# Kernel tuning notes

Measured on AMD Instinct MI355X. Metric: run time of the kernel, lower is better.

The kernel has to match this reference:

```python
import jax, jax.numpy as jnp
import numpy as np

KS = 3
K3 = KS ** 3
NUM_K = 4
KM_ITERS = 10  # fixed Lloyd iterations (original runs to tolerance)


def _unfold3d(xp, d, h, w):
    # xp: [B, C, d+2, h+2, w+2] -> [B, C, d, h, w, 27]; kernel dims flattened as (k1,k2,k3)
    sl = [xp[:, :, i:i + d, j:j + h, l:l + w]
          for i in range(KS) for j in range(KS) for l in range(KS)]
    return jnp.stack(sl, axis=-1)


def _kmeans(pts):
    # pts: [N, C]. Deterministic init with first NUM_K points, fixed Lloyd iterations.
    cent0 = pts[:NUM_K]

    def assign(cent):
        d2 = (jnp.sum(pts * pts, -1, keepdims=True)
              - 2.0 * (pts @ cent.T) + jnp.sum(cent * cent, -1))  # [N, K]
        return jnp.argmin(d2, axis=-1)

    def step(cent, _):
        oh = jax.nn.one_hot(assign(cent), NUM_K, dtype=pts.dtype)  # [N, K]
        cnt = jnp.maximum(oh.sum(0), 1.0)
        cent = (oh.T @ pts) / cnt[:, None]
        return cent, None

    cent, _ = jax.lax.scan(step, cent0, None, length=KM_ITERS)
    return assign(cent), cent


def _mlp3(z, w1, b1, w2, b2, w3, b3):
    z = jax.nn.relu(z @ w1 + b1)
    z = jax.nn.relu(z @ w2 + b2)
    return z @ w3 + b3


def reference(x, proj_w, base_w, gk_w1, gk_b1, gk_w2, gk_b2, gk_w3, gk_b3,
              gb_w1, gb_b1, gb_w2, gb_b2, gb_w3, gb_b3, prelu_a):
    b, c, d, h, w = x.shape
    o = base_w.shape[0]
    n = d * h * w
    x_in = x
    # 1x1x1 input projection (no bias)
    xp = jnp.einsum('oi,bidhw->bodhw', proj_w, x)
    xp = jnp.pad(xp, ((0, 0), (0, 0), (1, 1), (1, 1), (1, 1)))
    patches = _unfold3d(xp, d, h, w)                                # [b,c,d,h,w,27]
    # mean_type 's': mean over kernel dims -> per-voxel channel summary
    x_mean = patches.mean(-1).reshape(b, c, n).transpose(0, 2, 1)   # [b,n,c]
    idx, cent = jax.vmap(_kmeans)(x_mean)                           # [b,n], [b,K,c]
    feat = cent.reshape(b, NUM_K * c)
    # per-cluster dynamic kernel gates in (0,1)
    w_i = jax.nn.sigmoid(_mlp3(feat, gk_w1, gk_b1, gk_w2, gk_b2, gk_w3, gk_b3))
    w_i = w_i.reshape(b, NUM_K, K3).transpose(1, 0, 2)[:, :, None, None, :]  # [K,b,1,1,27]
    weight = (w_i * base_w).reshape(NUM_K, b, o, c * K3)            # [K,b,o,c*27]
    bias = _mlp3(feat, gb_w1, gb_b1, gb_w2, gb_b2, gb_w3, gb_b3)
    bias = bias.reshape(b, NUM_K, o).transpose(1, 0, 2)[..., None]  # [K,b,o,1]
    # im2col: [b, c*27, n] with (c, k) channel-major flattening as in the torch rearrange
    xf = patches.reshape(b, c, n, K3).transpose(0, 1, 3, 2).reshape(b, c * K3, n)
    out = jnp.einsum('kbof,bfn->kbon', weight, xf) + bias           # [K,b,o,n]
    mask = jax.nn.one_hot(idx, NUM_K, dtype=out.dtype)              # [b,n,K]
    out = (out * mask.transpose(2, 0, 1)[:, :, None, :]).sum(0)     # [b,o,n]
    out = out.reshape(b, o, d, h, w)
    out = jnp.where(out >= 0, out, prelu_a * out)                   # PReLU (single param)
    return out + x_in


def setup_inputs():
    key = jax.random.key(0)
    ks = jax.random.split(key, 12)
    B, C, O, D = 1, 64, 64, 40
    inner, inner2 = 128, 64
    fin = C * NUM_K

    def lin(k, i, o_):
        s = 1.0 / np.sqrt(i)
        return jax.random.uniform(k, (i, o_), jnp.float32, -s, s)

    return {
        'x': jax.random.normal(ks[0], (B, C, D, D, D), jnp.float32),
        'proj_w': jax.random.normal(ks[1], (C, C), jnp.float32) / np.sqrt(C),
        'base_w': jax.random.normal(ks[2], (O, C, K3), jnp.float32) / np.sqrt(C * K3),
        'gk_w1': lin(ks[3], fin, inner), 'gk_b1': jnp.zeros((inner,), jnp.float32),
        'gk_w2': lin(ks[4], inner, inner), 'gk_b2': jnp.zeros((inner,), jnp.float32),
        'gk_w3': lin(ks[5], inner, K3 * NUM_K), 'gk_b3': jnp.zeros((K3 * NUM_K,), jnp.float32),
        'gb_w1': lin(ks[6], fin, inner2), 'gb_b1': jnp.zeros((inner2,), jnp.float32),
        'gb_w2': lin(ks[7], inner2, inner2), 'gb_b2': jnp.zeros((inner2,), jnp.float32),
        'gb_w3': lin(ks[8], inner2, O * NUM_K), 'gb_b3': jnp.zeros((O * NUM_K,), jnp.float32),
        'prelu_a': jnp.full((1,), 0.25, jnp.float32),
    }
```

## Files before the change

kernel.cpp:

```cpp
#include <hip/hip_runtime.h>
#include <math.h>

typedef short v8s __attribute__((ext_vector_type(8)));
typedef float v4f __attribute__((ext_vector_type(4)));

#define NVOX 64000
#define NPAD 74088
#define P2   1764
#define GSTR 592704
#define NCPY 8
#define ITST (NCPY*260)

__device__ __forceinline__ unsigned short bf16rne(float f){
  unsigned int u = __float_as_uint(f);
  u += 0x7FFFu + ((u >> 16) & 1u);
  return (unsigned short)(u >> 16);
}

__global__ __launch_bounds__(256) void proj_k(const float* __restrict__ x,
                                              const float* __restrict__ pw,
                                              float* __restrict__ xp,
                                              short* __restrict__ xpt){
  int tid = threadIdx.x;
  int m = (blockIdx.x >> 1) * 256 + tid;
  int half = blockIdx.x & 1;
  float xv[64];
#pragma unroll
  for (int i = 0; i < 64; i++) xv[i] = x[(size_t)i * NVOX + m];
  int d = m / 1600; int r = m - d * 1600; int h = r / 40; int w = r - h * 40;
  int p = ((d + 1) * 42 + (h + 1)) * 42 + (w + 1);
  const float4* pw4 = (const float4*)pw;
  for (int g8 = half * 4; g8 < half * 4 + 4; g8++){
    v8s pk;
#pragma unroll
    for (int j = 0; j < 8; j++){
      int co = g8 * 8 + j;
      float acc = 0.f;
#pragma unroll
      for (int q = 0; q < 16; q++){
        float4 pv = pw4[co * 16 + q];
        acc = fmaf(pv.x, xv[4*q+0], acc);
        acc = fmaf(pv.y, xv[4*q+1], acc);
        acc = fmaf(pv.z, xv[4*q+2], acc);
        acc = fmaf(pv.w, xv[4*q+3], acc);
      }
      xp[(size_t)co * NVOX + m] = acc;
      pk[j] = (short)bf16rne(acc);
    }
    *(v8s*)(xpt + (size_t)g8 * GSTR + (size_t)p * 8) = pk;
  }
}

__global__ __launch_bounds__(256) void boxwh_k(const float* __restrict__ in,
                                               float* __restrict__ out){
  __shared__ float s0[1600], s1[1600];
  size_t base = (size_t)blockIdx.x * 1600;
  int t = threadIdx.x;
  for (int e = t; e < 1600; e += 256) s0[e] = in[base + e];
  __syncthreads();
  for (int e = t; e < 1600; e += 256){
    int w = e % 40;
    float s = s0[e];
    if (w > 0)  s += s0[e - 1];
    if (w < 39) s += s0[e + 1];
    s1[e] = s;
  }
  __syncthreads();
  for (int e = t; e < 1600; e += 256){
    int h = e / 40;
    float s = s1[e];
    if (h > 0)  s += s1[e - 40];
    if (h < 39) s += s1[e + 40];
    out[base + e] = s;
  }
}
__global__ void boxd_k(const float* __restrict__ in, float* __restrict__ out){
  int g = blockIdx.x * 256 + threadIdx.x;
  int d = (g / 1600) % 40;
  float s = in[g];
  if (d > 0)  s += in[g - 1600];
  if (d < 39) s += in[g + 1600];
  out[g] = s * (1.f / 27.f);
}

__global__ __launch_bounds__(256) void transp_k(const float* __restrict__ in,
                                                float* __restrict__ out){
  __shared__ float tile[64][65];
  int t = threadIdx.x;
  int nb = blockIdx.x * 64;
  int l = t & 63, g = t >> 6;
  for (int cc = g; cc < 64; cc += 4)
    tile[cc][l] = in[(size_t)cc * NVOX + nb + l];
  __syncthreads();
  for (int nn = g; nn < 64; nn += 4)
    out[(size_t)(nb + nn) * 64 + l] = tile[l][nn];
}

__global__ void kinit_k(const float* __restrict__ xmt, float* __restrict__ km){
  int t = threadIdx.x;
  km[t] = xmt[(size_t)(t >> 6) * 64 + (t & 63)];
  if (t < 4) km[256 + t] = 1.f;
  for (int j = 260 + t; j < 12 * ITST; j += 256) km[j] = 0.f;
}

__global__ __launch_bounds__(128) void assign_k(const float* __restrict__ xmt,
                                                const float* __restrict__ kin,
                                                float* __restrict__ kout,
                                                int* __restrict__ idx, int mode){
  __shared__ float s_cent[256];
  __shared__ float s_cc[4];
  __shared__ float s_red[260];
  __shared__ float s_x[128 * 65];
  __shared__ int   s_kb[128];
  int t = threadIdx.x, lane = t & 63, wv = t >> 6;
  for (int j = t; j < 256; j += 128){
    float sum = 0.f, cnt = 0.f;
#pragma unroll
    for (int s = 0; s < NCPY; s++){
      sum += kin[s * 260 + j];
      cnt += kin[s * 260 + 256 + (j >> 6)];
    }
    s_cent[j] = sum / fmaxf(cnt, 1.f);
  }
  for (int j = t; j < 260; j += 128) s_red[j] = 0.f;
  __syncthreads();
  if (t < 4){
    const float4* cc4 = (const float4*)(s_cent + t * 64);
    float s = 0.f;
#pragma unroll
    for (int q = 0; q < 16; q++){
      float4 v = cc4[q];
      s = fmaf(v.x, v.x, s); s = fmaf(v.y, v.y, s);
      s = fmaf(v.z, v.z, s); s = fmaf(v.w, v.w, s);
    }
    s_cc[t] = s;
  }
  __syncthreads();
  int n = blockIdx.x * 128 + t;
  const float4* xt = (const float4*)(xmt + (size_t)n * 64);
  float4 xq[16];
#pragma unroll
  for (int q = 0; q < 16; q++) xq[q] = xt[q];
  float d0 = 0.f, d1 = 0.f, d2 = 0.f, d3 = 0.f;
  const float4* c4 = (const float4*)s_cent;
#pragma unroll
  for (int q = 0; q < 16; q++){
    float4 p0 = c4[q], p1 = c4[16 + q], p2 = c4[32 + q], p3 = c4[48 + q];
    d0 = fmaf(p0.x, xq[q].x, d0); d0 = fmaf(p0.y, xq[q].y, d0);
    d0 = fmaf(p0.z, xq[q].z, d0); d0 = fmaf(p0.w, xq[q].w, d0);
    d1 = fmaf(p1.x, xq[q].x, d1); d1 = fmaf(p1.y, xq[q].y, d1);
    d1 = fmaf(p1.z, xq[q].z, d1); d1 = fmaf(p1.w, xq[q].w, d1);
    d2 = fmaf(p2.x, xq[q].x, d2); d2 = fmaf(p2.y, xq[q].y, d2);
    d2 = fmaf(p2.z, xq[q].z, d2); d2 = fmaf(p2.w, xq[q].w, d2);
    d3 = fmaf(p3.x, xq[q].x, d3); d3 = fmaf(p3.y, xq[q].y, d3);
    d3 = fmaf(p3.z, xq[q].z, d3); d3 = fmaf(p3.w, xq[q].w, d3);
  }
  float sc0 = s_cc[0] - 2.f * d0;
  float sc1 = s_cc[1] - 2.f * d1;
  float sc2 = s_cc[2] - 2.f * d2;
  float sc3 = s_cc[3] - 2.f * d3;
  int kb = 0; float bs = sc0;
  if (sc1 < bs){ bs = sc1; kb = 1; }
  if (sc2 < bs){ bs = sc2; kb = 2; }
  if (sc3 < bs){ bs = sc3; kb = 3; }
  if (mode){
    idx[n] = kb;
  } else {
    s_kb[t] = kb;
#pragma unroll
    for (int q = 0; q < 16; q++){
      s_x[t * 65 + 4*q + 0] = xq[q].x;
      s_x[t * 65 + 4*q + 1] = xq[q].y;
      s_x[t * 65 + 4*q + 2] = xq[q].z;
      s_x[t * 65 + 4*q + 3] = xq[q].w;
    }
    __syncthreads();
    float a0 = 0.f, a1 = 0.f, a2 = 0.f, a3 = 0.f;
    int rowbase = wv * 64;
#pragma unroll 16
    for (int j = 0; j < 64; j++){
      float v = s_x[(rowbase + j) * 65 + lane];
      int kj = s_kb[rowbase + j];
      a0 += (kj == 0) ? v : 0.f;
      a1 += (kj == 1) ? v : 0.f;
      a2 += (kj == 2) ? v : 0.f;
      a3 += (kj == 3) ? v : 0.f;
    }
    atomicAdd(&s_red[lane], a0);
    atomicAdd(&s_red[64 + lane], a1);
    atomicAdd(&s_red[128 + lane], a2);
    atomicAdd(&s_red[192 + lane], a3);
#pragma unroll
    for (int kk = 0; kk < 4; kk++){
      unsigned long long m = __ballot(kb == kk);
      if (lane == 0) atomicAdd(&s_red[256 + kk], (float)__popcll(m));
    }
    __syncthreads();
    float* kslot = kout + (blockIdx.x & (NCPY - 1)) * 260;
    for (int j = t; j < 260; j += 128) atomicAdd(&kslot[j], s_red[j]);
  }
}

__global__ void mlp_k(const float* __restrict__ km10,
                      const float* __restrict__ w1, const float* __restrict__ b1,
                      const float* __restrict__ w2, const float* __restrict__ b2,
                      const float* __restrict__ w3, const float* __restrict__ b3,
                      const float* __restrict__ u1, const float* __restrict__ c1,
                      const float* __restrict__ u2, const float* __restrict__ c2,
                      const float* __restrict__ u3, const float* __restrict__ c3,
                      float* __restrict__ wi, float* __restrict__ bias){
  __shared__ float s_feat[256], s_h1[128], s_h2[128], s_g1[64], s_g2[64];
  int t = threadIdx.x;
  {
    float sum = 0.f, cnt = 0.f;
#pragma unroll
    for (int s = 0; s < NCPY; s++){
      sum += km10[s * 260 + t];
      cnt += km10[s * 260 + 256 + (t >> 6)];
    }
    s_feat[t] = sum / fmaxf(cnt, 1.f);
  }
  __syncthreads();
  if (t < 128){
    float z = b1[t];
    for (int i = 0; i < 256; i++) z = fmaf(s_feat[i], w1[i * 128 + t], z);
    s_h1[t] = fmaxf(z, 0.f);
  }
  __syncthreads();
  if (t < 128){
    float z = b2[t];
    for (int i = 0; i < 128; i++) z = fmaf(s_h1[i], w2[i * 128 + t], z);
    s_h2[t] = fmaxf(z, 0.f);
  }
  __syncthreads();
  if (t < 108){
    float z = b3[t];
    for (int i = 0; i < 128; i++) z = fmaf(s_h2[i], w3[i * 108 + t], z);
    wi[t] = 1.f / (1.f + expf(-z));
  }
  if (t < 64){
    float z = c1[t];
    for (int i = 0; i < 256; i++) z = fmaf(s_feat[i], u1[i * 64 + t], z);
    s_g1[t] = fmaxf(z, 0.f);
  }
  __syncthreads();
  if (t < 64){
    float z = c2[t];
    for (int i = 0; i < 64; i++) z = fmaf(s_g1[i], u2[i * 64 + t], z);
    s_g2[t] = fmaxf(z, 0.f);
  }
  __syncthreads();
  {
    float z = c3[t];
    for (int i = 0; i < 64; i++) z = fmaf(s_g2[i], u3[i * 256 + t], z);
    bias[t] = z;
  }
}

__global__ void bwprep_k(const float* __restrict__ bw, short* __restrict__ bwb){
  int e = blockIdx.x * 256 + threadIdx.x;
  int t = e >> 12; int rem = e & 4095;
  int o = rem >> 6; int c = rem & 63;
  bwb[e] = (short)bf16rne(bw[(o * 64 + c) * 27 + t]);
}

__global__ __launch_bounds__(256) void conv_k(const short* __restrict__ xpt,
                                              const short* __restrict__ bwb,
                                              const float* __restrict__ wi,
                                              const float* __restrict__ bias,
                                              const int* __restrict__ idx,
                                              const float* __restrict__ x,
                                              const float* __restrict__ pa,
                                              float* __restrict__ out){
  static const int POFF[27] = {
    -P2-42-1, -P2-42, -P2-42+1, -P2-1, -P2, -P2+1, -P2+42-1, -P2+42, -P2+42+1,
    -42-1, -42, -42+1, -1, 0, 1, 42-1, 42, 42+1,
    P2-42-1, P2-42, P2-42+1, P2-1, P2, P2+1, P2+42-1, P2+42, P2+42+1 };
  __shared__ float s_wi[108];
  __shared__ float s_bias[256];
  __shared__ float s_acc[64 * 68];
  int tid = threadIdx.x;
  for (int j = tid; j < 108; j += 256) s_wi[j] = wi[j];
  s_bias[tid] = bias[tid];
  __syncthreads();
  int wv = tid >> 6, lane = tid & 63;
  int kc = wv & 1, mh = wv >> 1;
  int col = lane & 15, kg = lane >> 4;
  int vb = blockIdx.x * 64;
  int p4[4], ki4[4];
#pragma unroll
  for (int nt = 0; nt < 4; nt++){
    int v = vb + nt * 16 + col;
    ki4[nt] = idx[v];
    int d = v / 1600; int r = v - d * 1600; int h = r / 40; int w = r - h * 40;
    p4[nt] = ((d + 1) * 42 + (h + 1)) * 42 + (w + 1);
  }
  const short* bg = xpt + (size_t)(kc * 4 + kg) * GSTR;
  const short* bp0 = bg + (size_t)p4[0] * 8;
  const short* bp1 = bg + (size_t)p4[1] * 8;
  const short* bp2 = bg + (size_t)p4[2] * 8;
  const short* bp3 = bg + (size_t)p4[3] * 8;
  int ao0 = (mh * 32 + col) * 64 + kc * 32 + kg * 8;
  int ao1 = ao0 + 16 * 64;
  v4f acc[2][4];
#pragma unroll
  for (int m2 = 0; m2 < 2; m2++)
#pragma unroll
    for (int nt = 0; nt < 4; nt++) acc[m2][nt] = (v4f){0.f, 0.f, 0.f, 0.f};
  v4f zero = {0.f, 0.f, 0.f, 0.f};
#pragma unroll 9
  for (int t = 0; t < 27; t++){
    int po8 = POFF[t] * 8;
    v8s a0 = *(const v8s*)(bwb + t * 4096 + ao0);
    v8s a1 = *(const v8s*)(bwb + t * 4096 + ao1);
    v8s b0 = *(const v8s*)(bp0 + po8);
    v8s b1 = *(const v8s*)(bp1 + po8);
    v8s b2 = *(const v8s*)(bp2 + po8);
    v8s b3 = *(const v8s*)(bp3 + po8);
    float wk0 = s_wi[ki4[0] * 27 + t];
    float wk1 = s_wi[ki4[1] * 27 + t];
    float wk2 = s_wi[ki4[2] * 27 + t];
    float wk3 = s_wi[ki4[3] * 27 + t];
    v4f tp;
    tp = __builtin_amdgcn_mfma_f32_16x16x32_bf16(a0, b0, zero, 0, 0, 0); acc[0][0] += tp * wk0;
    tp = __builtin_amdgcn_mfma_f32_16x16x32_bf16(a1, b0, zero, 0, 0, 0); acc[1][0] += tp * wk0;
    tp = __builtin_amdgcn_mfma_f32_16x16x32_bf16(a0, b1, zero, 0, 0, 0); acc[0][1] += tp * wk1;
    tp = __builtin_amdgcn_mfma_f32_16x16x32_bf16(a1, b1, zero, 0, 0, 0); acc[1][1] += tp * wk1;
    tp = __builtin_amdgcn_mfma_f32_16x16x32_bf16(a0, b2, zero, 0, 0, 0); acc[0][2] += tp * wk2;
    tp = __builtin_amdgcn_mfma_f32_16x16x32_bf16(a1, b2, zero, 0, 0, 0); acc[1][2] += tp * wk2;
    tp = __builtin_amdgcn_mfma_f32_16x16x32_bf16(a0, b3, zero, 0, 0, 0); acc[0][3] += tp * wk3;
    tp = __builtin_amdgcn_mfma_f32_16x16x32_bf16(a1, b3, zero, 0, 0, 0); acc[1][3] += tp * wk3;
  }
  __syncthreads();
  if (kc == 1){
#pragma unroll
    for (int m2 = 0; m2 < 2; m2++)
#pragma unroll
      for (int nt = 0; nt < 4; nt++)
        *(v4f*)(&s_acc[(nt * 16 + col) * 68 + mh * 32 + m2 * 16 + kg * 4]) = acc[m2][nt];
  }
  __syncthreads();
  if (kc == 0){
    float pav = pa[0];
#pragma unroll
    for (int m2 = 0; m2 < 2; m2++){
#pragma unroll
      for (int nt = 0; nt < 4; nt++){
        v4f other = *(const v4f*)(&s_acc[(nt * 16 + col) * 68 + mh * 32 + m2 * 16 + kg * 4]);
        v4f sum = acc[m2][nt] + other;
        int n = vb + nt * 16 + col;
#pragma unroll
        for (int r = 0; r < 4; r++){
          int o = mh * 32 + m2 * 16 + kg * 4 + r;
          float val = sum[r] + s_bias[ki4[nt] * 64 + o];
          val = (val >= 0.f) ? val : pav * val;
          size_t off = (size_t)o * NVOX + n;
          out[off] = val + x[off];
        }
      }
    }
  }
}

extern "C" void kernel_launch(void* const* d_in, const int* in_sizes, int n_in,
                              void* d_out, int out_size, void* d_ws, size_t ws_size,
                              hipStream_t stream){
  const float* x    = (const float*)d_in[0];
  const float* pw   = (const float*)d_in[1];
  const float* bw   = (const float*)d_in[2];
  const float* gkw1 = (const float*)d_in[3];
  const float* gkb1 = (const float*)d_in[4];
  const float* gkw2 = (const float*)d_in[5];
  const float* gkb2 = (const float*)d_in[6];
  const float* gkw3 = (const float*)d_in[7];
  const float* gkb3 = (const float*)d_in[8];
  const float* gbw1 = (const float*)d_in[9];
  const float* gbb1 = (const float*)d_in[10];
  const float* gbw2 = (const float*)d_in[11];
  const float* gbb2 = (const float*)d_in[12];
  const float* gbw3 = (const float*)d_in[13];
  const float* gbb3 = (const float*)d_in[14];
  const float* pa   = (const float*)d_in[15];
  float* outp = (float*)d_out;

  float* ws   = (float*)d_ws;
  float* XP   = ws;
  float* BU2  = ws + 4096000;
  float* BU1  = ws + 8192000;
  short* XPT  = (short*)(ws + 12288000);
  short* BWB  = XPT + (size_t)NPAD * 64;
  float* KM   = (float*)(BWB + 110592);
  float* WI   = KM + 12 * ITST;
  float* BIAS = WI + 108;
  int*   IDX  = (int*)(BIAS + 256);
  float* XMT  = XP;

  hipMemsetAsync(XPT, 0, (size_t)NPAD * 64 * 2, stream);
  proj_k<<<500, 256, 0, stream>>>(x, pw, XP, XPT);
  boxwh_k<<<2560, 256, 0, stream>>>(XP, BU2);
  boxd_k<<<16000, 256, 0, stream>>>(BU2, BU1);
  transp_k<<<1000, 256, 0, stream>>>(BU1, XMT);
  kinit_k<<<1, 256, 0, stream>>>(XMT, KM);
  for (int i = 0; i <= 10; i++)
    assign_k<<<500, 128, 0, stream>>>(XMT, KM + i * ITST, KM + (i + 1) * ITST, IDX,
                                      (i == 10) ? 1 : 0);
  mlp_k<<<1, 256, 0, stream>>>(KM + 10 * ITST,
                               gkw1, gkb1, gkw2, gkb2, gkw3, gkb3,
                               gbw1, gbb1, gbw2, gbb2, gbw3, gbb3,
                               WI, BIAS);
  bwprep_k<<<432, 256, 0, stream>>>(bw, BWB);
  conv_k<<<1000, 256, 0, stream>>>(XPT, BWB, WI, BIAS, IDX, x, pa, outp);
}
```

Before: 332.9 us.

## Fuse k-means init and Lloyd iterations into one cooperative persistent kernel

Replaces the init kernel and the eleven separate assign launches with a single cooperative kernel of 250 blocks of 256 threads. Each thread keeps its voxel feature vector in registers and in shared memory across all iterations, and grid.sync replaces the kernel-launch boundaries between iterations. This removes per-launch overhead and the repeated reload of the point data from global memory. In exchange it uses a large shared-memory tile of about 67 KB per block, which limits occupancy. It also relies on every block being co-resident for the grid-wide barrier to work.

```diff
diff --git a/kernel.cpp b/kernel.cpp
--- a/kernel.cpp
+++ b/kernel.cpp
@@ -1,5 +1,8 @@
 #include <hip/hip_runtime.h>
+#include <hip/hip_cooperative_groups.h>
 #include <math.h>
+
+namespace cg = cooperative_groups;
 
 typedef short v8s __attribute__((ext_vector_type(8)));
 typedef float v4f __attribute__((ext_vector_type(4)));
@@ -96,108 +99,114 @@
     out[(size_t)(nb + nn) * 64 + l] = tile[l][nn];
 }
 
-__global__ void kinit_k(const float* __restrict__ xmt, float* __restrict__ km){
-  int t = threadIdx.x;
-  km[t] = xmt[(size_t)(t >> 6) * 64 + (t & 63)];
-  if (t < 4) km[256 + t] = 1.f;
-  for (int j = 260 + t; j < 12 * ITST; j += 256) km[j] = 0.f;
-}
-
-__global__ __launch_bounds__(128) void assign_k(const float* __restrict__ xmt,
-                                                const float* __restrict__ kin,
-                                                float* __restrict__ kout,
-                                                int* __restrict__ idx, int mode){
+__global__ __launch_bounds__(256) void kmeans_k(const float* __restrict__ xmt,
+                                                float* __restrict__ km,
+                                                int* __restrict__ idx){
+  cg::grid_group grid = cg::this_grid();
   __shared__ float s_cent[256];
   __shared__ float s_cc[4];
   __shared__ float s_red[260];
-  __shared__ float s_x[128 * 65];
-  __shared__ int   s_kb[128];
+  __shared__ float s_x[256 * 65];
+  __shared__ int   s_kb[256];
   int t = threadIdx.x, lane = t & 63, wv = t >> 6;
-  for (int j = t; j < 256; j += 128){
-    float sum = 0.f, cnt = 0.f;
-#pragma unroll
-    for (int s = 0; s < NCPY; s++){
-      sum += kin[s * 260 + j];
-      cnt += kin[s * 260 + 256 + (j >> 6)];
-    }
-    s_cent[j] = sum / fmaxf(cnt, 1.f);
-  }
-  for (int j = t; j < 260; j += 128) s_red[j] = 0.f;
-  __syncthreads();
-  if (t < 4){
-    const float4* cc4 = (const float4*)(s_cent + t * 64);
-    float s = 0.f;
-#pragma unroll
-    for (int q = 0; q < 16; q++){
-      float4 v = cc4[q];
-      s = fmaf(v.x, v.x, s); s = fmaf(v.y, v.y, s);
-      s = fmaf(v.z, v.z, s); s = fmaf(v.w, v.w, s);
-    }
-    s_cc[t] = s;
-  }
-  __syncthreads();
-  int n = blockIdx.x * 128 + t;
+  int n = blockIdx.x * 256 + t;
+
+  for (int j = 260 + n; j < 12 * ITST; j += 250 * 256) km[j] = 0.f;
+  if (blockIdx.x == 0){
+    km[t] = xmt[(size_t)(t >> 6) * 64 + (t & 63)];
+    if (t < 4) km[256 + t] = 1.f;
+  }
+
   const float4* xt = (const float4*)(xmt + (size_t)n * 64);
   float4 xq[16];
 #pragma unroll
   for (int q = 0; q < 16; q++) xq[q] = xt[q];
-  float d0 = 0.f, d1 = 0.f, d2 = 0.f, d3 = 0.f;
-  const float4* c4 = (const float4*)s_cent;
 #pragma unroll
   for (int q = 0; q < 16; q++){
-    float4 p0 = c4[q], p1 = c4[16 + q], p2 = c4[32 + q], p3 = c4[48 + q];
-    d0 = fmaf(p0.x, xq[q].x, d0); d0 = fmaf(p0.y, xq[q].y, d0);
-    d0 = fmaf(p0.z, xq[q].z, d0); d0 = fmaf(p0.w, xq[q].w, d0);
-    d1 = fmaf(p1.x, xq[q].x, d1); d1 = fmaf(p1.y, xq[q].y, d1);
-    d1 = fmaf(p1.z, xq[q].z, d1); d1 = fmaf(p1.w, xq[q].w, d1);
-    d2 = fmaf(p2.x, xq[q].x, d2); d2 = fmaf(p2.y, xq[q].y, d2);
-    d2 = fmaf(p2.z, xq[q].z, d2); d2 = fmaf(p2.w, xq[q].w, d2);
-    d3 = fmaf(p3.x, xq[q].x, d3); d3 = fmaf(p3.y, xq[q].y, d3);
-    d3 = fmaf(p3.z, xq[q].z, d3); d3 = fmaf(p3.w, xq[q].w, d3);
-  }
-  float sc0 = s_cc[0] - 2.f * d0;
-  float sc1 = s_cc[1] - 2.f * d1;
-  float sc2 = s_cc[2] - 2.f * d2;
-  float sc3 = s_cc[3] - 2.f * d3;
-  int kb = 0; float bs = sc0;
-  if (sc1 < bs){ bs = sc1; kb = 1; }
-  if (sc2 < bs){ bs = sc2; kb = 2; }
-  if (sc3 < bs){ bs = sc3; kb = 3; }
-  if (mode){
-    idx[n] = kb;
-  } else {
-    s_kb[t] = kb;
+    s_x[t * 65 + 4*q + 0] = xq[q].x;
+    s_x[t * 65 + 4*q + 1] = xq[q].y;
+    s_x[t * 65 + 4*q + 2] = xq[q].z;
+    s_x[t * 65 + 4*q + 3] = xq[q].w;
+  }
+  grid.sync();
+
+  for (int iter = 0; iter <= 10; ++iter){
+    const float* kin = km + iter * ITST;
+    {
+      float sum = 0.f, cnt = 0.f;
+#pragma unroll
+      for (int s = 0; s < NCPY; s++){
+        sum += kin[s * 260 + t];
+        cnt += kin[s * 260 + 256 + (t >> 6)];
+      }
+      s_cent[t] = sum / fmaxf(cnt, 1.f);
+    }
+    for (int j = t; j < 260; j += 256) s_red[j] = 0.f;
+    __syncthreads();
+    if (t < 4){
+      const float4* cc4 = (const float4*)(s_cent + t * 64);
+      float s = 0.f;
+#pragma unroll
+      for (int q = 0; q < 16; q++){
+        float4 v = cc4[q];
+        s = fmaf(v.x, v.x, s); s = fmaf(v.y, v.y, s);
+        s = fmaf(v.z, v.z, s); s = fmaf(v.w, v.w, s);
+      }
+      s_cc[t] = s;
+    }
+    __syncthreads();
+    float d0 = 0.f, d1 = 0.f, d2 = 0.f, d3 = 0.f;
+    const float4* c4 = (const float4*)s_cent;
 #pragma unroll
     for (int q = 0; q < 16; q++){
-      s_x[t * 65 + 4*q + 0] = xq[q].x;
-      s_x[t * 65 + 4*q + 1] = xq[q].y;
-      s_x[t * 65 + 4*q + 2] = xq[q].z;
-      s_x[t * 65 + 4*q + 3] = xq[q].w;
-    }
-    __syncthreads();
-    float a0 = 0.f, a1 = 0.f, a2 = 0.f, a3 = 0.f;
-    int rowbase = wv * 64;
+      float4 p0 = c4[q], p1 = c4[16 + q], p2 = c4[32 + q], p3 = c4[48 + q];
+      d0 = fmaf(p0.x, xq[q].x, d0); d0 = fmaf(p0.y, xq[q].y, d0);
+      d0 = fmaf(p0.z, xq[q].z, d0); d0 = fmaf(p0.w, xq[q].w, d0);
+      d1 = fmaf(p1.x, xq[q].x, d1); d1 = fmaf(p1.y, xq[q].y, d1);
+      d1 = fmaf(p1.z, xq[q].z, d1); d1 = fmaf(p1.w, xq[q].w, d1);
+      d2 = fmaf(p2.x, xq[q].x, d2); d2 = fmaf(p2.y, xq[q].y, d2);
+      d2 = fmaf(p2.z, xq[q].z, d2); d2 = fmaf(p2.w, xq[q].w, d2);
+      d3 = fmaf(p3.x, xq[q].x, d3); d3 = fmaf(p3.y, xq[q].y, d3);
+      d3 = fmaf(p3.z, xq[q].z, d3); d3 = fmaf(p3.w, xq[q].w, d3);
+    }
+    float sc0 = s_cc[0] - 2.f * d0;
+    float sc1 = s_cc[1] - 2.f * d1;
+    float sc2 = s_cc[2] - 2.f * d2;
+    float sc3 = s_cc[3] - 2.f * d3;
+    int kb = 0; float bs = sc0;
+    if (sc1 < bs){ bs = sc1; kb = 1; }
+    if (sc2 < bs){ bs = sc2; kb = 2; }
+    if (sc3 < bs){ bs = sc3; kb = 3; }
+    if (iter == 10){
+      idx[n] = kb;
+    } else {
+      s_kb[t] = kb;
+      __syncthreads();
+      float a0 = 0.f, a1 = 0.f, a2 = 0.f, a3 = 0.f;
+      int rowbase = wv * 64;
 #pragma unroll 16
-    for (int j = 0; j < 64; j++){
-      float v = s_x[(rowbase + j) * 65 + lane];
-      int kj = s_kb[rowbase + j];
-      a0 += (kj == 0) ? v : 0.f;
-      a1 += (kj == 1) ? v : 0.f;
-      a2 += (kj == 2) ? v : 0.f;
-      a3 += (kj == 3) ? v : 0.f;
-    }
-    atomicAdd(&s_red[lane], a0);
-    atomicAdd(&s_red[64 + lane], a1);
-    atomicAdd(&s_red[128 + lane], a2);
-    atomicAdd(&s_red[192 + lane], a3);
-#pragma unroll
-    for (int kk = 0; kk < 4; kk++){
-      unsigned long long m = __ballot(kb == kk);
-      if (lane == 0) atomicAdd(&s_red[256 + kk], (float)__popcll(m));
-    }
-    __syncthreads();
-    float* kslot = kout + (blockIdx.x & (NCPY - 1)) * 260;
-    for (int j = t; j < 260; j += 128) atomicAdd(&kslot[j], s_red[j]);
+      for (int j = 0; j < 64; j++){
+        float v = s_x[(rowbase + j) * 65 + lane];
+        int kj = s_kb[rowbase + j];
+        a0 += (kj == 0) ? v : 0.f;
+        a1 += (kj == 1) ? v : 0.f;
+        a2 += (kj == 2) ? v : 0.f;
+        a3 += (kj == 3) ? v : 0.f;
+      }
+      atomicAdd(&s_red[lane], a0);
+      atomicAdd(&s_red[64 + lane], a1);
+      atomicAdd(&s_red[128 + lane], a2);
+      atomicAdd(&s_red[192 + lane], a3);
+#pragma unroll
+      for (int kk = 0; kk < 4; kk++){
+        unsigned long long m = __ballot(kb == kk);
+        if (lane == 0) atomicAdd(&s_red[256 + kk], (float)__popcll(m));
+      }
+      __syncthreads();
+      float* kslot = km + (iter + 1) * ITST + (blockIdx.x & (NCPY - 1)) * 260;
+      for (int j = t; j < 260; j += 256) atomicAdd(&kslot[j], s_red[j]);
+      grid.sync();
+    }
   }
 }
 
@@ -400,10 +409,11 @@
   boxwh_k<<<2560, 256, 0, stream>>>(XP, BU2);
   boxd_k<<<16000, 256, 0, stream>>>(BU2, BU1);
   transp_k<<<1000, 256, 0, stream>>>(BU1, XMT);
-  kinit_k<<<1, 256, 0, stream>>>(XMT, KM);
-  for (int i = 0; i <= 10; i++)
-    assign_k<<<500, 128, 0, stream>>>(XMT, KM + i * ITST, KM + (i + 1) * ITST, IDX,
-                                      (i == 10) ? 1 : 0);
+  {
+    const float* xmt_p = XMT; float* km_p = KM; int* idx_p = IDX;
+    void* kargs[] = { (void*)&xmt_p, (void*)&km_p, (void*)&idx_p };
+    hipLaunchCooperativeKernel((void*)kmeans_k, dim3(250), dim3(256), kargs, 0, stream);
+  }
   mlp_k<<<1, 256, 0, stream>>>(KM + 10 * ITST,
                                gkw1, gkb1, gkw2, gkb2, gkw3, gkb3,
                                gbw1, gbb1, gbw2, gbb2, gbw3, gbb3,
```

After: 637.0 us. 91.4% more time.
